# Kernel tuning notes

Hardware: AMD Instinct MI355X
Metric: run time of the kernel (lower is better)

The kernel has to match this reference:

```python
import jax, jax.numpy as jnp
import jax.scipy.linalg as jsp
import numpy as np

# Problem dimensions (match init_kwargs P_shape/A_shape)
N = 256   # variables
M = 512   # constraints
B = 64    # batch

# OSQP ADMM hyper-parameters (fixed-rho variant of the OSQP algorithm)
SIGMA = 1e-6
RHO = 0.1
ALPHA = 1.6
N_ITERS = 500


def setup_inputs() -> dict:
    key = jax.random.key(0)
    kP, kq, kA, kc = jax.random.split(key, 4)
    # P is diagonal with strictly positive entries -> PSD (values are the nnz of P)
    P_val = jax.random.uniform(kP, (B, N), dtype=jnp.float32) + 0.1
    q_val = jax.random.normal(kq, (B, N), dtype=jnp.float32)
    # A is a dense pattern; values stored row-major as its nnz vector
    A_val = jax.random.normal(kA, (B, M * N), dtype=jnp.float32) / np.sqrt(N)
    # Feasible box: l <= u by construction
    center = jax.random.normal(kc, (B, M), dtype=jnp.float32)
    l_val = center - 1.0
    u_val = center + 1.0
    return {"P_val": P_val, "q_val": q_val, "A_val": A_val, "l_val": l_val, "u_val": u_val}


def _admm_qp(P_val, q_val, A_val, l_val, u_val):
    """Batched OSQP-style ADMM solve of min 1/2 x'Px + q'x  s.t. l <= Ax <= u.

    P is diagonal (nnz pattern = diag), A is dense (nnz pattern = full m x n).
    """
    A = A_val.reshape(B, M, N)                      # [B,m,n]
    # KKT-like matrix M_k = P + sigma*I + rho*A'A   [B,n,n]
    eye = jnp.eye(N, dtype=P_val.dtype)
    P_diag = P_val + SIGMA                          # diagonal of P + sigma*I
    Mk = RHO * jnp.einsum('bmi,bmj->bij', A, A) + jax.vmap(jnp.diag)(P_diag)
    L = jnp.linalg.cholesky(Mk)                     # [B,n,n], factor once, reuse
    Lt = jnp.swapaxes(L, -1, -2)

    def kkt_solve(rhs):                             # rhs [B,n]
        y1 = jsp.solve_triangular(L, rhs[..., None], lower=True)
        y2 = jsp.solve_triangular(Lt, y1, lower=False)
        return y2[..., 0]

    x0 = jnp.zeros((B, N), dtype=P_val.dtype)
    z0 = jnp.zeros((B, M), dtype=P_val.dtype)
    y0 = jnp.zeros((B, M), dtype=P_val.dtype)

    def step(state, _):
        x, z, y = state
        rhs = SIGMA * x - q_val + jnp.einsum('bmn,bm->bn', A, RHO * z - y)
        x_t = kkt_solve(rhs)                        # x-tilde
        z_t = jnp.einsum('bmn,bn->bm', A, x_t)      # z-tilde = A x_t
        x_new = ALPHA * x_t + (1.0 - ALPHA) * x
        z_hat = ALPHA * z_t + (1.0 - ALPHA) * z
        z_new = jnp.clip(z_hat + y / RHO, l_val, u_val)
        y_new = y + RHO * (z_hat - z_new)
        return (x_new, z_new, y_new), None

    (x, _, _), _ = jax.lax.scan(step, (x0, z0, y0), None, length=N_ITERS)
    return x


def reference(P_val, q_val, A_val, l_val, u_val):
    return _admm_qp(P_val, q_val, A_val, l_val, u_val)   # [B, n] primal solutions
```

## Files before the change

### kernel.cpp

```cpp
#include <hip/hip_runtime.h>
#include <hip/hip_fp16.h>

#define N_VAR 256
#define M_CON 512
#define BATCH 64
#define SIGMA_C 1e-6f
#define RHO_C 0.1f
#define ALPHA_C 1.6f
#define NITERS 500

__global__ __launch_bounds__(256) void k_transpose(const float* __restrict__ A,
                                                   float* __restrict__ At) {
  __shared__ float tile[32][33];
  int b = blockIdx.z;
  int n0 = blockIdx.x * 32;
  int m0 = blockIdx.y * 32;
  const float* Ab = A + (size_t)b * (M_CON * N_VAR);
  float* Atb = At + (size_t)b * (M_CON * N_VAR);
  int tx = threadIdx.x, ty = threadIdx.y;
#pragma unroll
  for (int j = 0; j < 32; j += 8)
    tile[ty + j][tx] = Ab[(size_t)(m0 + ty + j) * N_VAR + n0 + tx];
  __syncthreads();
#pragma unroll
  for (int j = 0; j < 32; j += 8)
    Atb[(size_t)(n0 + ty + j) * M_CON + m0 + tx] = tile[tx][ty + j];
}

__global__ __launch_bounds__(256) void k_ntgemm(
    const float* __restrict__ X, const float* __restrict__ Y,
    float* __restrict__ C, int I, int J, int K,
    long long bsX, long long bsY, long long bsC, float alpha,
    const float* __restrict__ diagv, int tilesJ) {
  int b = blockIdx.y;
  int ti = blockIdx.x / tilesJ, tj = blockIdx.x % tilesJ;
  int i0 = ti * 128, j0 = tj * 128;
  const float* Xb = X + (size_t)b * bsX;
  const float* Yb = Y + (size_t)b * bsY;
  float* Cb = C + (size_t)b * bsC;
  __shared__ float Xs[16][128];
  __shared__ float Ys[16][128];
  int tid = threadIdx.x;
  int tx = tid & 15, ty = tid >> 4;
  float acc[8][8];
#pragma unroll
  for (int r = 0; r < 8; ++r)
#pragma unroll
    for (int c = 0; c < 8; ++c) acc[r][c] = 0.0f;

  for (int kk = 0; kk < K; kk += 16) {
#pragma unroll
    for (int v = 0; v < 2; ++v) {
      int idx = v * 256 + tid;
      int row = idx >> 2;
      int k4 = (idx & 3) * 4;
      float4 gx = *(const float4*)(Xb + (size_t)(i0 + row) * K + kk + k4);
      Xs[k4 + 0][row] = gx.x; Xs[k4 + 1][row] = gx.y;
      Xs[k4 + 2][row] = gx.z; Xs[k4 + 3][row] = gx.w;
      float4 gy = *(const float4*)(Yb + (size_t)(j0 + row) * K + kk + k4);
      Ys[k4 + 0][row] = gy.x; Ys[k4 + 1][row] = gy.y;
      Ys[k4 + 2][row] = gy.z; Ys[k4 + 3][row] = gy.w;
    }
    __syncthreads();
#pragma unroll
    for (int k = 0; k < 16; ++k) {
      float xr[8], yr[8];
      *(float4*)&xr[0] = *(float4*)&Xs[k][ty * 8];
      *(float4*)&xr[4] = *(float4*)&Xs[k][ty * 8 + 4];
      *(float4*)&yr[0] = *(float4*)&Ys[k][tx * 8];
      *(float4*)&yr[4] = *(float4*)&Ys[k][tx * 8 + 4];
#pragma unroll
      for (int r = 0; r < 8; ++r)
#pragma unroll
        for (int c = 0; c < 8; ++c) acc[r][c] += xr[r] * yr[c];
    }
    __syncthreads();
  }
#pragma unroll
  for (int r = 0; r < 8; ++r) {
    int gi = i0 + ty * 8 + r;
#pragma unroll
    for (int c = 0; c < 8; ++c) {
      int gj = j0 + tx * 8 + c;
      float val = acc[r][c] * alpha;
      if (diagv != nullptr && gi == gj) val += diagv[(size_t)b * N_VAR + gi] + SIGMA_C;
      Cb[(size_t)gi * J + gj] = val;
    }
  }
}

__global__ __launch_bounds__(512, 2) void k_invert(const float* __restrict__ Mk,
                                                   float* __restrict__ Mi) {
  int b = blockIdx.x;
  const float* src = Mk + (size_t)b * 65536;
  float* dst = Mi + (size_t)b * 65536;
  int t = threadIdx.x;
  int c = t & 255, rh = t >> 8;

  float a[128];
#pragma unroll
  for (int j = 0; j < 128; ++j) a[j] = src[(size_t)(rh * 128 + j) * 256 + c];

  __shared__ float colPan[256][8];
  __shared__ float rowPan[2][8][260];
  __shared__ float PiSh[64];
  __shared__ float Rp[8][260];

  int rh_s = __builtin_amdgcn_readfirstlane(rh);
  int cw_s = __builtin_amdgcn_readfirstlane((t >> 6) & 3);

  if (rh == 0) {
#pragma unroll
    for (int j = 0; j < 8; ++j) rowPan[0][j][c] = a[j];
  }
  __syncthreads();

  for (int s = 0; s < 32; ++s) {
    int kb = s * 8;
    int cur = s & 1, nxt = cur ^ 1;
    int kh = kb >> 7, kj = kb & 127;
    int khn = (kb + 8) >> 7, kjn = (kb + 8) & 127;
    bool mycol = (c >= kb) && (c < kb + 8);

    if (cw_s == (kb >> 6)) {
      if (mycol) {
        int f = c - kb;
#pragma unroll
        for (int j = 0; j < 128; ++j) colPan[rh * 128 + j][f] = a[j];
      }
    }
    if (t < 64) {
      int e = t >> 3, f = t & 7;
      float p = rowPan[cur][e][kb + f];
#pragma unroll
      for (int k2 = 0; k2 < 8; ++k2) {
        float piv = __shfl(p, k2 * 8 + k2);
        float rv = __shfl(p, k2 * 8 + f);
        float cv = __shfl(p, e * 8 + k2);
        float pivinv = 1.0f / piv;
        float srv = rv * pivinv;
        float gen = p - cv * srv;
        p = gen;
        if (e == k2) p = srv;
        if (f == k2) p = -cv * pivinv;
        if (e == k2 && f == k2) p = pivinv;
      }
      PiSh[t] = p;
    }
    __syncthreads();

    float rpan[8];
#pragma unroll
    for (int f2 = 0; f2 < 8; ++f2) rpan[f2] = rowPan[cur][f2][c];
    float rp[8];
#pragma unroll
    for (int e = 0; e < 8; ++e) {
      float4 p0 = *(const float4*)&PiSh[e * 8];
      float4 p1 = *(const float4*)&PiSh[e * 8 + 4];
      rp[e] = p0.x * rpan[0] + p0.y * rpan[1] + p0.z * rpan[2] + p0.w * rpan[3] +
              p1.x * rpan[4] + p1.y * rpan[5] + p1.z * rpan[6] + p1.w * rpan[7];
    }
    if (cw_s == (kb >> 6)) {
      if (mycol) {
        int f = c - kb;
#pragma unroll
        for (int e = 0; e < 8; ++e) rp[e] = PiSh[e * 8 + f];
      }
    }
#pragma unroll
    for (int e = 0; e < 8; ++e) Rp[e][c] = rp[e];

    bool myhalfk = (rh_s == kh);
    bool stashw = (s != 31) && (rh_s == khn);
#pragma unroll
    for (int j = 0; j < 128; ++j) {
      float4 c0 = *(const float4*)&colPan[rh * 128 + j][0];
      float4 c1 = *(const float4*)&colPan[rh * 128 + j][4];
      float aold = a[j];
      float nv = aold -
                 (c0.x * rp[0] + c0.y * rp[1] + c0.z * rp[2] + c0.w * rp[3] +
                  c1.x * rp[4] + c1.y * rp[5] + c1.z * rp[6] + c1.w * rp[7]);
      if (mycol) nv -= aold;
      if (myhalfk && j >= kj && j < kj + 8)
        nv = Rp[j - kj][c];
      a[j] = nv;
      if (stashw && j >= kjn && j < kjn + 8)
        rowPan[nxt][j - kjn][c] = nv;
    }
    __syncthreads();
  }

#pragma unroll
  for (int j = 0; j < 128; ++j) dst[(size_t)(rh * 128 + j) * 256 + c] = a[j];
}

__global__ __launch_bounds__(256) void k_matvec_h(const float* __restrict__ Mi,
                                                  const float* __restrict__ q,
                                                  float* __restrict__ h) {
  int b = blockIdx.x, t = threadIdx.x;
  __shared__ float qs[256];
  qs[t] = q[(size_t)b * 256 + t];
  __syncthreads();
  const float* Mb = Mi + (size_t)b * 65536;
  float acc = 0.0f;
  for (int k = 0; k < 256; ++k) acc += Mb[(size_t)k * 256 + t] * qs[k];
  h[(size_t)b * 256 + t] = acc;
}

__global__ __launch_bounds__(512) void k_matvec_d(const float* __restrict__ At,
                                                  const float* __restrict__ h,
                                                  float* __restrict__ d) {
  int b = blockIdx.x, t = threadIdx.x;
  __shared__ float hs[256];
  if (t < 256) hs[t] = h[(size_t)b * 256 + t];
  __syncthreads();
  const float* Ab = At + (size_t)b * 131072;
  float acc = 0.0f;
  for (int n = 0; n < 256; ++n) acc += Ab[(size_t)n * 512 + t] * hs[n];
  d[(size_t)b * 512 + t] = acc;
}

__global__ __launch_bounds__(512, 2) void k_admm4(
    const float* __restrict__ G, const float* __restrict__ dvec,
    const float* __restrict__ lv, const float* __restrict__ uv,
    unsigned long long* __restrict__ wtag, float* __restrict__ Sbuf) {
  int g = blockIdx.x;
  int b = (g & 7) + 8 * ((g >> 3) & 7);
  int s = g >> 6;
  int t = threadIdx.x;
  int l = t & 63, wv = t >> 6;
  int c0 = wv * 64;

  __shared__ __align__(16) float wloc[512];
  __shared__ float part[8][128];

  const float* Gb = G + (size_t)b * 262144;
  const float* g0p = Gb + (size_t)(s * 128 + l) * 512 + c0;
  const float* g1p = Gb + (size_t)(s * 128 + 64 + l) * 512 + c0;
  float G0[64], G1[64];
#pragma unroll
  for (int j = 0; j < 16; ++j) {
    float4 v0 = *(const float4*)(g0p + 4 * j);
    G0[4 * j + 0] = v0.x; G0[4 * j + 1] = v0.y;
    G0[4 * j + 2] = v0.z; G0[4 * j + 3] = v0.w;
    float4 v1 = *(const float4*)(g1p + 4 * j);
    G1[4 * j + 0] = v1.x; G1[4 * j + 1] = v1.y;
    G1[4 * j + 2] = v1.z; G1[4 * j + 3] = v1.w;
  }

  float zreg = 0.0f, yreg = 0.0f, Sreg = 0.0f;
  float lreg = 0.0f, ureg = 0.0f, dreg = 0.0f;
  if (t < 128) {
    lreg = lv[(size_t)b * 512 + s * 128 + t];
    ureg = uv[(size_t)b * 512 + s * 128 + t];
    dreg = dvec[(size_t)b * 512 + s * 128 + t];
  }
  wloc[t] = 0.0f;

  unsigned long long* wt0 = wtag + (size_t)b * 512;
  unsigned long long* wt1 = wtag + 32768 + (size_t)b * 512;
  int gr = (s * 128 + t) & 511;
  const float4* wq4 = (const float4*)(wloc + c0);

  for (int it = 0; it < NITERS; ++it) {
    __syncthreads();

    float r0a = 0.f, r0b = 0.f, r1a = 0.f, r1b = 0.f;
#pragma unroll
    for (int j = 0; j < 8; ++j) {
      float4 wa = wq4[2 * j];
      float4 wc = wq4[2 * j + 1];
      r0a += G0[8 * j + 0] * wa.x + G0[8 * j + 1] * wa.y +
             G0[8 * j + 2] * wa.z + G0[8 * j + 3] * wa.w;
      r1a += G1[8 * j + 0] * wa.x + G1[8 * j + 1] * wa.y +
             G1[8 * j + 2] * wa.z + G1[8 * j + 3] * wa.w;
      r0b += G0[8 * j + 4] * wc.x + G0[8 * j + 5] * wc.y +
             G0[8 * j + 6] * wc.z + G0[8 * j + 7] * wc.w;
      r1b += G1[8 * j + 4] * wc.x + G1[8 * j + 5] * wc.y +
             G1[8 * j + 6] * wc.z + G1[8 * j + 7] * wc.w;
    }
    part[wv][l] = r0a + r0b;
    part[wv][64 + l] = r1a + r1b;
    __syncthreads();

    if (t < 128) {
      float w_old = RHO_C * zreg - yreg;
      Sreg = w_old - 0.6f * Sreg;
      float p = part[0][t] + part[1][t] + part[2][t] + part[3][t] +
                part[4][t] + part[5][t] + part[6][t] + part[7][t];
      float zt = p - dreg;
      float zh = ALPHA_C * zt + (1.0f - ALPHA_C) * zreg;
      float zc = zh + yreg * (1.0f / RHO_C);
      zc = fminf(fmaxf(zc, lreg), ureg);
      yreg += RHO_C * (zh - zc);
      zreg = zc;
      float wn = RHO_C * zreg - yreg;
      wloc[s * 128 + t] = wn;
      if (it < NITERS - 1) {
        unsigned long long pk =
            ((unsigned long long)(unsigned)(it + 1) << 32) |
            (unsigned long long)__float_as_uint(wn);
        unsigned long long* wp = ((it + 1) & 1) ? wt1 : wt0;
        __hip_atomic_store(&wp[s * 128 + t], pk, __ATOMIC_RELAXED,
                           __HIP_MEMORY_SCOPE_AGENT);
      }
    } else if (it < NITERS - 1) {
      unsigned long long* wp = ((it + 1) & 1) ? wt1 : wt0;
      unsigned want = (unsigned)(it + 1);
      unsigned long long v;
      for (;;) {
        v = __hip_atomic_load(&wp[gr], __ATOMIC_RELAXED,
                              __HIP_MEMORY_SCOPE_AGENT);
        if ((unsigned)(v >> 32) == want) break;
        __builtin_amdgcn_s_sleep(1);
      }
      wloc[gr] = __uint_as_float((unsigned)(v & 0xffffffffu));
    }
  }

  if (t < 128) Sbuf[(size_t)b * 512 + s * 128 + t] = Sreg;
}

__global__ __launch_bounds__(256) void k_final(
    const float* __restrict__ A, const float* __restrict__ q,
    const float* __restrict__ Mi, const float* __restrict__ Sbuf,
    float* __restrict__ xout) {
  int b = blockIdx.x, t = threadIdx.x;
  __shared__ float Ssh[512];
  __shared__ float uu[256];
  for (int i = t; i < 512; i += 256) Ssh[i] = Sbuf[(size_t)b * 512 + i];
  __syncthreads();
  const float* Ab = A + (size_t)b * 131072;
  float acc = 0.0f;
  for (int m = 0; m < 512; ++m) acc += Ab[(size_t)m * 256 + t] * Ssh[m];
  uu[t] = ALPHA_C * acc - q[(size_t)b * 256 + t];
  __syncthreads();
  const float* Mb = Mi + (size_t)b * 65536;
  float x = 0.0f;
  for (int kk = 0; kk < 256; ++kk) x += Mb[(size_t)kk * 256 + t] * uu[kk];
  xout[(size_t)b * 256 + t] = x;
}

extern "C" void kernel_launch(void* const* d_in, const int* in_sizes, int n_in,
                              void* d_out, int out_size, void* d_ws, size_t ws_size,
                              hipStream_t stream) {
  (void)in_sizes; (void)n_in; (void)out_size; (void)ws_size;
  const float* P = (const float*)d_in[0];
  const float* q = (const float*)d_in[1];
  const float* Av = (const float*)d_in[2];
  const float* lv = (const float*)d_in[3];
  const float* uv = (const float*)d_in[4];
  float* xout = (float*)d_out;

  float* ws = (float*)d_ws;
  float* At = ws;
  float* F  = ws;
  float* Mi = ws + 8388608;
  float* Mk = ws + 12582912;
  float* G  = ws + 12582912;
  float* hv = ws + 29360128;
  float* dv = ws + 29376512;
  float* Sbuf = ws + 29409280;
  unsigned long long* wtag = (unsigned long long*)ws;

  k_transpose<<<dim3(8, 16, 64), dim3(32, 8), 0, stream>>>(Av, At);
  k_ntgemm<<<dim3(4, 64), 256, 0, stream>>>(At, At, Mk, 256, 256, 512,
                                            131072LL, 131072LL, 65536LL,
                                            RHO_C, P, 2);
  k_invert<<<64, 512, 0, stream>>>(Mk, Mi);
  k_matvec_h<<<64, 256, 0, stream>>>(Mi, q, hv);
  k_matvec_d<<<64, 512, 0, stream>>>(At, hv, dv);
  k_ntgemm<<<dim3(8, 64), 256, 0, stream>>>(Av, Mi, F, 512, 256, 256,
                                            131072LL, 65536LL, 131072LL,
                                            1.0f, nullptr, 2);
  k_ntgemm<<<dim3(16, 64), 256, 0, stream>>>(F, Av, G, 512, 512, 256,
                                             131072LL, 131072LL, 262144LL,
                                             1.0f, nullptr, 4);
  k_admm4<<<256, 512, 0, stream>>>(G, dv, lv, uv, wtag, Sbuf);
  k_final<<<64, 256, 0, stream>>>(Av, q, Mi, Sbuf, xout);
}
```

Baseline: 1.643 ms.

## Replace per-iteration block barrier with per-wave polling of peer tags

Each wave now polls the global tagged slots for exactly the 64 w entries it consumes and writes them into a wave-private LDS slice. This removes the leading __syncthreads, so each wave can begin its mat-vec as soon as its own inputs arrive instead of waiting on the whole block. The partial-sum buffer is double-buffered so the single remaining barrier per iteration stays safe. The trade-off is that all 512 threads now spin on global atomics, including the block's own 128 locally produced values, which previously came straight from LDS. That adds memory polling traffic and latency on the block's own data.

Result: faster. 1.592 ms (-3.1%).

```diff
diff --git a/kernel.cpp b/kernel.cpp
--- a/kernel.cpp
+++ b/kernel.cpp
@@ -231,8 +231,8 @@
   int l = t & 63, wv = t >> 6;
   int c0 = wv * 64;
 
-  __shared__ __align__(16) float wloc[512];
-  __shared__ float part[8][128];
+  __shared__ __align__(16) float wbuf[8][64];
+  __shared__ float part[2][8][128];
 
   const float* Gb = G + (size_t)b * 262144;
   const float* g0p = Gb + (size_t)(s * 128 + l) * 512 + c0;
@@ -255,15 +255,25 @@
     ureg = uv[(size_t)b * 512 + s * 128 + t];
     dreg = dvec[(size_t)b * 512 + s * 128 + t];
   }
-  wloc[t] = 0.0f;
+  wbuf[wv][l] = 0.0f;
 
   unsigned long long* wt0 = wtag + (size_t)b * 512;
   unsigned long long* wt1 = wtag + 32768 + (size_t)b * 512;
-  int gr = (s * 128 + t) & 511;
-  const float4* wq4 = (const float4*)(wloc + c0);
+  const float4* wq4 = (const float4*)(wbuf[wv]);
 
   for (int it = 0; it < NITERS; ++it) {
-    __syncthreads();
+    if (it > 0) {
+      unsigned long long* wp = (it & 1) ? wt1 : wt0;
+      unsigned want = (unsigned)it;
+      unsigned long long v;
+      for (;;) {
+        v = __hip_atomic_load(&wp[c0 + l], __ATOMIC_RELAXED,
+                              __HIP_MEMORY_SCOPE_AGENT);
+        if (__all((unsigned)(v >> 32) == want)) break;
+        __builtin_amdgcn_s_sleep(1);
+      }
+      wbuf[wv][l] = __uint_as_float((unsigned)(v & 0xffffffffu));
+    }
 
     float r0a = 0.f, r0b = 0.f, r1a = 0.f, r1b = 0.f;
 #pragma unroll
@@ -279,24 +289,25 @@
       r1b += G1[8 * j + 4] * wc.x + G1[8 * j + 5] * wc.y +
              G1[8 * j + 6] * wc.z + G1[8 * j + 7] * wc.w;
     }
-    part[wv][l] = r0a + r0b;
-    part[wv][64 + l] = r1a + r1b;
+    int pp = it & 1;
+    part[pp][wv][l] = r0a + r0b;
+    part[pp][wv][64 + l] = r1a + r1b;
     __syncthreads();
 
     if (t < 128) {
       float w_old = RHO_C * zreg - yreg;
       Sreg = w_old - 0.6f * Sreg;
-      float p = part[0][t] + part[1][t] + part[2][t] + part[3][t] +
-                part[4][t] + part[5][t] + part[6][t] + part[7][t];
+      float p = part[pp][0][t] + part[pp][1][t] + part[pp][2][t] +
+                part[pp][3][t] + part[pp][4][t] + part[pp][5][t] +
+                part[pp][6][t] + part[pp][7][t];
       float zt = p - dreg;
       float zh = ALPHA_C * zt + (1.0f - ALPHA_C) * zreg;
       float zc = zh + yreg * (1.0f / RHO_C);
       zc = fminf(fmaxf(zc, lreg), ureg);
       yreg += RHO_C * (zh - zc);
       zreg = zc;
-      float wn = RHO_C * zreg - yreg;
-      wloc[s * 128 + t] = wn;
       if (it < NITERS - 1) {
+        float wn = RHO_C * zreg - yreg;
         unsigned long long pk =
             ((unsigned long long)(unsigned)(it + 1) << 32) |
             (unsigned long long)__float_as_uint(wn);
@@ -304,17 +315,6 @@
         __hip_atomic_store(&wp[s * 128 + t], pk, __ATOMIC_RELAXED,
                            __HIP_MEMORY_SCOPE_AGENT);
       }
-    } else if (it < NITERS - 1) {
-      unsigned long long* wp = ((it + 1) & 1) ? wt1 : wt0;
-      unsigned want = (unsigned)(it + 1);
-      unsigned long long v;
-      for (;;) {
-        v = __hip_atomic_load(&wp[gr], __ATOMIC_RELAXED,
-                              __HIP_MEMORY_SCOPE_AGENT);
-        if ((unsigned)(v >> 32) == want) break;
-        __builtin_amdgcn_s_sleep(1);
-      }
-      wloc[gr] = __uint_as_float((unsigned)(v & 0xffffffffu));
     }
   }
 
```
